# Kernel tuning notes

Hardware: AMD Instinct MI355X
Metric: run time of the kernel (lower is better)

The kernel has to match this reference:

```python
import jax, jax.numpy as jnp
import numpy as np

B = 2048          # number of drug pairs (graphs)
N_PER_DRUG = 32   # nodes per drug subgraph (uniform for static shapes)
F = 128           # node_feature_dim
H = 128           # hidden_dim
E = 1048576       # total edges (~avg degree 8 per node)


def setup_inputs() -> dict:
    key = jax.random.key(0)
    ks = jax.random.split(key, 12)
    total = B * 2 * N_PER_DRUG
    x = jax.random.normal(ks[0], (total, F), dtype=jnp.float32)
    # edges generated within each drug subgraph (2B blocks of N_PER_DRUG nodes)
    blk = jax.random.randint(ks[1], (E,), 0, 2 * B)
    src = blk * N_PER_DRUG + jax.random.randint(ks[2], (E,), 0, N_PER_DRUG)
    dst = blk * N_PER_DRUG + jax.random.randint(ks[3], (E,), 0, N_PER_DRUG)
    edge_index = jnp.stack([src, dst]).astype(jnp.int32)
    ptr = (jnp.arange(B + 1) * 2 * N_PER_DRUG).astype(jnp.int32)
    split = jnp.full((B,), N_PER_DRUG, dtype=jnp.int32)

    def lin(k, shape, fan_in):
        return jax.random.normal(k, shape, dtype=jnp.float32) * (1.0 / np.sqrt(fan_in))

    return {
        "x": x, "edge_index": edge_index, "ptr": ptr, "split": split,
        "W1": lin(ks[4], (F, H), F), "b1": jnp.zeros((H,), jnp.float32),
        "W2": lin(ks[5], (H, H), H), "b2": jnp.zeros((H,), jnp.float32),
        "Wm1": lin(ks[6], (2 * H, H), 2 * H), "bm1": jnp.zeros((H,), jnp.float32),
        "Wm2": lin(ks[7], (H, 1), H), "bm2": jnp.zeros((1,), jnp.float32),
    }


def reference(x, edge_index, ptr, split, W1, b1, W2, b2, Wm1, bm1, Wm2, bm2):
    num_nodes = x.shape[0]
    nB = ptr.shape[0] - 1
    idx = jnp.arange(num_nodes, dtype=jnp.int32)
    g = (jnp.searchsorted(ptr, idx, side="right") - 1).astype(jnp.int32)
    local = idx - ptr[g]
    drug = (local >= split[g]).astype(jnp.int32)
    seg = 2 * g + drug                      # (graph, drug-half) segment id
    src, dst = edge_index[0], edge_index[1]
    # edge valid iff same graph AND same drug half (== the per-sample masks)
    w = (seg[src] == seg[dst]).astype(x.dtype)
    # GCN normalization with self-loops (shared by both layers)
    deg = jax.ops.segment_sum(w, dst, num_segments=num_nodes) + 1.0
    dinv = jax.lax.rsqrt(deg)
    norm = dinv[src] * dinv[dst] * w        # [E]
    self_norm = (dinv * dinv)[:, None]      # [N,1]

    def gcn(h, W, b):
        hw = h @ W
        agg = jax.ops.segment_sum(norm[:, None] * hw[src], dst, num_segments=num_nodes)
        return agg + self_norm * hw + b

    h = jax.nn.relu(gcn(x, W1, b1))
    h = jax.nn.relu(gcn(h, W2, b2))
    nseg = 2 * nB
    cnt = jax.ops.segment_sum(jnp.ones((num_nodes,), x.dtype), seg, num_segments=nseg)
    pooled = jax.ops.segment_sum(h, seg, num_segments=nseg) / jnp.maximum(cnt, 1.0)[:, None]
    pair = jnp.concatenate([pooled[0::2], pooled[1::2]], axis=1)  # [B, 2H]
    z = jax.nn.relu(pair @ Wm1 + bm1) @ Wm2 + bm2
    return jax.nn.sigmoid(z).reshape(-1)
```

## Files before the change

### kernel.cpp

```cpp
#include <hip/hip_runtime.h>
#include <hip/hip_bf16.h>
#include <math.h>

#define NF 128
#define ECAP 512

typedef short bf16x8 __attribute__((ext_vector_type(8)));
typedef float f32x4  __attribute__((ext_vector_type(4)));

union U8 { unsigned u[4]; bf16x8 v; };

__device__ __forceinline__ unsigned pk2(float lo, float hi) {
    union { __hip_bfloat162 h2; unsigned u; } c;
    c.h2 = __float22bfloat162_rn(make_float2(lo, hi));
    return c.u;
}
__device__ __forceinline__ unsigned short f2bf(float f) {
    union { __hip_bfloat16 h; unsigned short u; } c;
    c.h = __float2bfloat16(f);
    return c.u;
}

__global__ void k_prep(const int* __restrict__ ptr, const int* __restrict__ split,
                       int nB, int N, int nseg,
                       unsigned* __restrict__ segloc, int* __restrict__ segstart,
                       int* __restrict__ segcnt, int* __restrict__ cursor,
                       const float* __restrict__ W1, const float* __restrict__ W2,
                       short* __restrict__ Wt1, short* __restrict__ Wt2) {
    int i = blockIdx.x * blockDim.x + threadIdx.x;
    if (i < N) {
        int lo = 0, hi = nB + 1;
        while (lo < hi) { int mid = (lo + hi) >> 1; if (ptr[mid] <= i) lo = mid + 1; else hi = mid; }
        int g = lo - 1;
        int local = i - ptr[g];
        int sp = split[g];
        int drug = (local >= sp) ? 1 : 0;
        int seg = 2 * g + drug;
        int loc = local - (drug ? sp : 0);
        segloc[i] = ((unsigned)seg << 8) | (unsigned)loc;
    }
    if (i < nseg) {
        int g = i >> 1;
        int base = ptr[g];
        int sp = split[g];
        segstart[i] = (i & 1) ? base + sp : base;
        segcnt[i]   = (i & 1) ? (ptr[g + 1] - base - sp) : sp;
        cursor[i]   = 0;
    }
    if (i < 32768) {
        int m = i >> 14;
        int rem = i & 16383;
        int n = rem & 127;
        int k = rem >> 7;
        const float* W = m ? W2 : W1;
        short* Wt = m ? Wt2 : Wt1;
        Wt[n * 128 + k] = (short)f2bf(W[k * 128 + n]);
    }
}

__global__ void __launch_bounds__(1024) k_sort(
    const int* __restrict__ src, const int* __restrict__ dst, int E, int nseg,
    const unsigned* __restrict__ segloc, int* __restrict__ cursor,
    unsigned short* __restrict__ ebuf)
{
    __shared__ unsigned cnt[4096];
    __shared__ unsigned gbase[4096];
    const int t  = threadIdx.x;
    const int e0 = blockIdx.x * 4096;

    for (int i = t; i < 4096; i += 1024) cnt[i] = 0;
    __syncthreads();

    unsigned code[4];
    #pragma unroll
    for (int k = 0; k < 4; ++k) {
        int e = e0 + k * 1024 + t;
        code[k] = 0xFFFFFFFFu;
        if (e < E) {
            unsigned ss = segloc[src[e]], dd = segloc[dst[e]];
            if ((ss >> 8) == (dd >> 8)) {
                code[k] = ((ss >> 8) << 12) | ((dd & 63u) << 6) | (ss & 63u);
                atomicAdd(&cnt[ss >> 8], 1u);
            }
        }
    }
    __syncthreads();

    for (int i = t; i < nseg; i += 1024) {
        unsigned c = cnt[i];
        if (c) gbase[i] = (unsigned)atomicAdd(&cursor[i], (int)c);
    }
    __syncthreads();
    for (int i = t; i < 4096; i += 1024) cnt[i] = 0;
    __syncthreads();

    #pragma unroll
    for (int k = 0; k < 4; ++k) {
        if (code[k] != 0xFFFFFFFFu) {
            unsigned s = code[k] >> 12;
            unsigned pos = gbase[s] + atomicAdd(&cnt[s], 1u);
            if (pos < ECAP)
                ebuf[(s << 9) + pos] = (unsigned short)(code[k] & 0xFFFu);
        }
    }
}

__global__ void __launch_bounds__(64, 3) k_gcn5(
    const float* __restrict__ x,
    const int* __restrict__ segstart, const int* __restrict__ segcnt,
    const int* __restrict__ ecnt, const unsigned short* __restrict__ ebuf,
    const short* __restrict__ Wt1, const float* __restrict__ b1,
    const short* __restrict__ Wt2, const float* __restrict__ b2,
    float* __restrict__ pooled)
{
    __shared__ short xt[128 * 40];
    float* Afp = (float*)xt;
    short* zb  = xt;

    const int seg = blockIdx.x;
    const int l  = threadIdx.x;
    const int fr = l & 15;
    const int g  = l >> 4;
    const int swz = (fr & 7) << 3;

    const int start = segstart[seg];
    const int cnt   = segcnt[seg];

    const int f0 = (l & 7) * 16;
    const int c0 = (l >> 3) * 4;
    float xr[4][16];
    #pragma unroll
    for (int i = 0; i < 4; ++i) {
        if (c0 + i < cnt) {
            const float4* rp = (const float4*)(x + (size_t)(start + c0 + i) * NF + f0);
            float4 a = rp[0], b = rp[1], c = rp[2], d = rp[3];
            xr[i][0]=a.x; xr[i][1]=a.y; xr[i][2]=a.z; xr[i][3]=a.w;
            xr[i][4]=b.x; xr[i][5]=b.y; xr[i][6]=b.z; xr[i][7]=b.w;
            xr[i][8]=c.x; xr[i][9]=c.y; xr[i][10]=c.z; xr[i][11]=c.w;
            xr[i][12]=d.x; xr[i][13]=d.y; xr[i][14]=d.z; xr[i][15]=d.w;
        } else {
            #pragma unroll
            for (int j = 0; j < 16; ++j) xr[i][j] = 0.f;
        }
    }

    for (int i = l; i < 1088; i += 64) Afp[i] = 0.f;
    __syncthreads();

    {
        int en = ecnt[seg];
        en = en < ECAP ? en : ECAP;
        const unsigned short* eb = ebuf + ((size_t)seg << 9);
        for (int i = l; i < en; i += 64) {
            unsigned c = eb[i];
            if ((c & ((32u << 6) | 32u)) == 0u)
                atomicAdd(&Afp[((c >> 6) & 31) * 33 + (c & 31)], 1.0f);
        }
    }
    __syncthreads();

    {
        int r = l & 31, half = l >> 5;
        float s = 0.f;
        const float* row = &Afp[r * 33 + half * 16];
        #pragma unroll
        for (int k = 0; k < 16; ++k) s += row[k];
        s += __shfl_xor(s, 32);
        float dv = rsqrtf(1.0f + s);
        if (l < 32) Afp[1056 + r] = dv;
    }
    __syncthreads();

    bf16x8 bfr0, bfr1;
    {
        float dr0 = Afp[1056 + fr];
        float dr1 = Afp[1056 + 16 + fr];
        float e0[8], e1[8];
        #pragma unroll
        for (int j = 0; j < 8; ++j) {
            int c = g * 8 + j;
            float dc = Afp[1056 + c];
            float v0 = Afp[fr * 33 + c]        * dr0 * dc;
            float v1 = Afp[(16 + fr) * 33 + c] * dr1 * dc;
            if (fr == c)      v0 += dr0 * dr0;
            if (16 + fr == c) v1 += dr1 * dr1;
            e0[j] = v0; e1[j] = v1;
        }
        U8 u0, u1;
        u0.u[0] = pk2(e0[0], e0[1]); u0.u[1] = pk2(e0[2], e0[3]);
        u0.u[2] = pk2(e0[4], e0[5]); u0.u[3] = pk2(e0[6], e0[7]);
        u1.u[0] = pk2(e1[0], e1[1]); u1.u[1] = pk2(e1[2], e1[3]);
        u1.u[2] = pk2(e1[4], e1[5]); u1.u[3] = pk2(e1[6], e1[7]);
        bfr0 = u0.v; bfr1 = u1.v;
    }
    __syncthreads();

    #pragma unroll
    for (int j = 0; j < 16; ++j) {
        uint2 w;
        w.x = pk2(xr[0][j], xr[1][j]);
        w.y = pk2(xr[2][j], xr[3][j]);
        *reinterpret_cast<uint2*>(&xt[(f0 + j) * 40 + c0]) = w;
    }
    __syncthreads();

    for (int layer = 0; layer < 2; ++layer) {
        const short* Wt = layer ? Wt2 : Wt1;
        const float* bb = layer ? b2  : b1;

        unsigned zp[8][4];
        __builtin_amdgcn_s_setprio(1);
        #pragma unroll
        for (int mt = 0; mt < 8; ++mt) {
            bf16x8 af = *(const bf16x8*)&xt[(mt * 16 + fr) * 40 + g * 8];
            f32x4 z0 = {0.f, 0.f, 0.f, 0.f};
            f32x4 z1 = {0.f, 0.f, 0.f, 0.f};
            z0 = __builtin_amdgcn_mfma_f32_16x16x32_bf16(af, bfr0, z0, 0, 0, 0);
            z1 = __builtin_amdgcn_mfma_f32_16x16x32_bf16(af, bfr1, z1, 0, 0, 0);
            zp[mt][0] = pk2(z0[0], z0[1]); zp[mt][1] = pk2(z0[2], z0[3]);
            zp[mt][2] = pk2(z1[0], z1[1]); zp[mt][3] = pk2(z1[2], z1[3]);
        }
        __builtin_amdgcn_s_setprio(0);
        __syncthreads();

        #pragma unroll
        for (int mt = 0; mt < 8; ++mt) {
            int fb = mt * 16 + 4 * g;
            uint2 w0, w1;
            w0.x = zp[mt][0]; w0.y = zp[mt][1];
            w1.x = zp[mt][2]; w1.y = zp[mt][3];
            *reinterpret_cast<uint2*>(&zb[fr * 128 + (fb ^ swz)])        = w0;
            *reinterpret_cast<uint2*>(&zb[(16 + fr) * 128 + (fb ^ swz)]) = w1;
        }
        __syncthreads();

        f32x4 acc[2][8];
        #pragma unroll
        for (int i = 0; i < 2; ++i)
            #pragma unroll
            for (int j = 0; j < 8; ++j) acc[i][j] = (f32x4){0.f, 0.f, 0.f, 0.f};
        #pragma unroll
        for (int kk = 0; kk < 4; ++kk) {
            const int ko = kk * 32 + g * 8;
            bf16x8 a0 = *(const bf16x8*)&zb[fr * 128 + (ko ^ swz)];
            bf16x8 a1 = *(const bf16x8*)&zb[(16 + fr) * 128 + (ko ^ swz)];
            __builtin_amdgcn_s_setprio(1);
            #pragma unroll
            for (int nt = 0; nt < 8; ++nt) {
                bf16x8 wf = *(const bf16x8*)&Wt[(nt * 16 + fr) * 128 + ko];
                acc[0][nt] = __builtin_amdgcn_mfma_f32_16x16x32_bf16(a0, wf, acc[0][nt], 0, 0, 0);
                acc[1][nt] = __builtin_amdgcn_mfma_f32_16x16x32_bf16(a1, wf, acc[1][nt], 0, 0, 0);
            }
            __builtin_amdgcn_s_setprio(0);
        }

        if (layer == 0) {
            __syncthreads();
            #pragma unroll
            for (int nt = 0; nt < 8; ++nt) {
                float bv = bb[nt * 16 + fr];
                #pragma unroll
                for (int mt = 0; mt < 2; ++mt) {
                    float h0 = acc[mt][nt][0] + bv; h0 = h0 > 0.f ? h0 : 0.f;
                    float h1 = acc[mt][nt][1] + bv; h1 = h1 > 0.f ? h1 : 0.f;
                    float h2 = acc[mt][nt][2] + bv; h2 = h2 > 0.f ? h2 : 0.f;
                    float h3 = acc[mt][nt][3] + bv; h3 = h3 > 0.f ? h3 : 0.f;
                    uint2 w;
                    w.x = pk2(h0, h1); w.y = pk2(h2, h3);
                    *reinterpret_cast<uint2*>(&xt[(nt * 16 + fr) * 40 + mt * 16 + 4 * g]) = w;
                }
            }
            __syncthreads();
        } else {
            float rcpc = 1.0f / (float)(cnt > 0 ? cnt : 1);
            #pragma unroll
            for (int nt = 0; nt < 8; ++nt) {
                float bv = bb[nt * 16 + fr];
                float pm = 0.f;
                #pragma unroll
                for (int mt = 0; mt < 2; ++mt)
                    #pragma unroll
                    for (int r = 0; r < 4; ++r) {
                        int node = mt * 16 + 4 * g + r;
                        float h = acc[mt][nt][r] + bv;
                        h = h > 0.f ? h : 0.f;
                        if (node < cnt) pm += h;
                    }
                pm += __shfl_xor(pm, 16);
                pm += __shfl_xor(pm, 32);
                if (l < 16) pooled[(size_t)seg * NF + nt * 16 + l] = pm * rcpc;
            }
        }
    }
}

__global__ void __launch_bounds__(128) k_mlp(
    const float* __restrict__ pooled, const float* __restrict__ Wm1,
    const float* __restrict__ bm1, const float* __restrict__ Wm2,
    const float* __restrict__ bm2, float* __restrict__ out, int nB) {
    __shared__ float pr[4][256];
    __shared__ float red[4][2];
    const int b0 = blockIdx.x * 4;
    const int t = threadIdx.x;

    for (int i = t; i < 1024; i += 128) {
        int p = i >> 8, c = i & 255;
        int pair = b0 + p;
        pr[p][c] = (pair < nB) ? pooled[(size_t)(2 * pair + (c >> 7)) * 128 + (c & 127)] : 0.f;
    }
    __syncthreads();

    float acc0 = bm1[t], acc1 = acc0, acc2 = acc0, acc3 = acc0;
    #pragma unroll 4
    for (int k = 0; k < 256; ++k) {
        float w = Wm1[k * 128 + t];
        acc0 += pr[0][k] * w;
        acc1 += pr[1][k] * w;
        acc2 += pr[2][k] * w;
        acc3 += pr[3][k] * w;
    }
    float wm2 = Wm2[t];
    float v[4];
    v[0] = (acc0 > 0.f ? acc0 : 0.f) * wm2;
    v[1] = (acc1 > 0.f ? acc1 : 0.f) * wm2;
    v[2] = (acc2 > 0.f ? acc2 : 0.f) * wm2;
    v[3] = (acc3 > 0.f ? acc3 : 0.f) * wm2;
    #pragma unroll
    for (int p = 0; p < 4; ++p) {
        #pragma unroll
        for (int o = 32; o > 0; o >>= 1) v[p] += __shfl_xor(v[p], o);
    }
    if ((t & 63) == 0) {
        int w = t >> 6;
        red[0][w] = v[0]; red[1][w] = v[1]; red[2][w] = v[2]; red[3][w] = v[3];
    }
    __syncthreads();
    if (t < 4 && b0 + t < nB) {
        float z = red[t][0] + red[t][1] + bm2[0];
        out[b0 + t] = 1.f / (1.f + expf(-z));
    }
}

static inline size_t alup(size_t v) { return (v + 255) & ~(size_t)255; }

extern "C" void kernel_launch(void* const* d_in, const int* in_sizes, int n_in,
                              void* d_out, int out_size, void* d_ws, size_t ws_size,
                              hipStream_t stream) {
    const float* x     = (const float*)d_in[0];
    const int*   edge  = (const int*)d_in[1];
    const int*   ptr   = (const int*)d_in[2];
    const int*   split = (const int*)d_in[3];
    const float* W1  = (const float*)d_in[4];
    const float* b1  = (const float*)d_in[5];
    const float* W2  = (const float*)d_in[6];
    const float* b2  = (const float*)d_in[7];
    const float* Wm1 = (const float*)d_in[8];
    const float* bm1 = (const float*)d_in[9];
    const float* Wm2 = (const float*)d_in[10];
    const float* bm2 = (const float*)d_in[11];
    float* out = (float*)d_out;

    const int N    = in_sizes[0] / NF;
    const int E    = in_sizes[1] / 2;
    const int nB   = in_sizes[2] - 1;
    const int nseg = 2 * nB;

    char* ws = (char*)d_ws;
    size_t off = 0;
    unsigned*       segloc   = (unsigned*)(ws + off);       off += alup((size_t)N * 4);
    int*            segstart = (int*)(ws + off);            off += alup((size_t)nseg * 4);
    int*            segcnt   = (int*)(ws + off);            off += alup((size_t)nseg * 4);
    int*            cursor   = (int*)(ws + off);            off += alup((size_t)nseg * 4);
    unsigned short* ebuf     = (unsigned short*)(ws + off); off += alup((size_t)nseg * ECAP * 2);
    float*          pooled   = (float*)(ws + off);          off += alup((size_t)nseg * NF * 4);
    short*          Wt1      = (short*)(ws + off);          off += alup(128 * 128 * 2);
    short*          Wt2      = (short*)(ws + off);          off += alup(128 * 128 * 2);

    const int* srcp = edge;
    const int* dstp = edge + E;

    int prepN = N > 32768 ? N : 32768;
    if (prepN < nseg) prepN = nseg;

    k_prep<<<(prepN + 255) / 256, 256, 0, stream>>>(ptr, split, nB, N, nseg,
                                                    segloc, segstart, segcnt, cursor,
                                                    W1, W2, Wt1, Wt2);
    k_sort<<<(E + 4095) / 4096, 1024, 0, stream>>>(srcp, dstp, E, nseg, segloc, cursor, ebuf);
    k_gcn5<<<nseg, 64, 0, stream>>>(x, segstart, segcnt, cursor, ebuf,
                                    Wt1, b1, Wt2, b2, pooled);
    k_mlp<<<(nB + 3) / 4, 128, 0, stream>>>(pooled, Wm1, bm1, Wm2, bm2, out, nB);
}
```

Before: 222.1 us.

## Build per-segment packed 4-bit adjacency via global atomics; split GCN over two waves

After: 241.3 us. 1.09x slower.

```diff
diff --git a/kernel.cpp b/kernel.cpp
--- a/kernel.cpp
+++ b/kernel.cpp
@@ -3,7 +3,6 @@
 #include <math.h>
 
 #define NF 128
-#define ECAP 512
 
 typedef short bf16x8 __attribute__((ext_vector_type(8)));
 typedef float f32x4  __attribute__((ext_vector_type(4)));
@@ -24,7 +23,7 @@
 __global__ void k_prep(const int* __restrict__ ptr, const int* __restrict__ split,
                        int nB, int N, int nseg,
                        unsigned* __restrict__ segloc, int* __restrict__ segstart,
-                       int* __restrict__ segcnt, int* __restrict__ cursor,
+                       int* __restrict__ segcnt,
                        const float* __restrict__ W1, const float* __restrict__ W2,
                        short* __restrict__ Wt1, short* __restrict__ Wt2) {
     int i = blockIdx.x * blockDim.x + threadIdx.x;
@@ -45,7 +44,6 @@
         int sp = split[g];
         segstart[i] = (i & 1) ? base + sp : base;
         segcnt[i]   = (i & 1) ? (ptr[g + 1] - base - sp) : sp;
-        cursor[i]   = 0;
     }
     if (i < 32768) {
         int m = i >> 14;
@@ -58,67 +56,33 @@
     }
 }
 
-__global__ void __launch_bounds__(1024) k_sort(
-    const int* __restrict__ src, const int* __restrict__ dst, int E, int nseg,
-    const unsigned* __restrict__ segloc, int* __restrict__ cursor,
-    unsigned short* __restrict__ ebuf)
-{
-    __shared__ unsigned cnt[4096];
-    __shared__ unsigned gbase[4096];
-    const int t  = threadIdx.x;
-    const int e0 = blockIdx.x * 4096;
-
-    for (int i = t; i < 4096; i += 1024) cnt[i] = 0;
-    __syncthreads();
-
-    unsigned code[4];
-    #pragma unroll
-    for (int k = 0; k < 4; ++k) {
-        int e = e0 + k * 1024 + t;
-        code[k] = 0xFFFFFFFFu;
-        if (e < E) {
-            unsigned ss = segloc[src[e]], dd = segloc[dst[e]];
-            if ((ss >> 8) == (dd >> 8)) {
-                code[k] = ((ss >> 8) << 12) | ((dd & 63u) << 6) | (ss & 63u);
-                atomicAdd(&cnt[ss >> 8], 1u);
-            }
-        }
-    }
-    __syncthreads();
-
-    for (int i = t; i < nseg; i += 1024) {
-        unsigned c = cnt[i];
-        if (c) gbase[i] = (unsigned)atomicAdd(&cursor[i], (int)c);
-    }
-    __syncthreads();
-    for (int i = t; i < 4096; i += 1024) cnt[i] = 0;
-    __syncthreads();
-
-    #pragma unroll
-    for (int k = 0; k < 4; ++k) {
-        if (code[k] != 0xFFFFFFFFu) {
-            unsigned s = code[k] >> 12;
-            unsigned pos = gbase[s] + atomicAdd(&cnt[s], 1u);
-            if (pos < ECAP)
-                ebuf[(s << 9) + pos] = (unsigned short)(code[k] & 0xFFFu);
-        }
-    }
-}
-
-__global__ void __launch_bounds__(64, 3) k_gcn5(
+__global__ void k_cnt(const int* __restrict__ src, const int* __restrict__ dst, int E,
+                      const unsigned* __restrict__ segloc, unsigned* __restrict__ Abits) {
+    int e = blockIdx.x * blockDim.x + threadIdx.x;
+    if (e >= E) return;
+    unsigned ss = segloc[src[e]], dd = segloc[dst[e]];
+    if ((ss >> 8) == (dd >> 8) && ((ss | dd) & 0xE0u) == 0u) {
+        unsigned eidx = (dd & 31u) * 32u + (ss & 31u);
+        atomicAdd(&Abits[(ss >> 8) * 128u + (eidx >> 3)], 1u << (4u * (eidx & 7u)));
+    }
+}
+
+__global__ void __launch_bounds__(128, 6) k_gcn6(
     const float* __restrict__ x,
     const int* __restrict__ segstart, const int* __restrict__ segcnt,
-    const int* __restrict__ ecnt, const unsigned short* __restrict__ ebuf,
+    const unsigned* __restrict__ Abits,
     const short* __restrict__ Wt1, const float* __restrict__ b1,
     const short* __restrict__ Wt2, const float* __restrict__ b2,
     float* __restrict__ pooled)
 {
     __shared__ short xt[128 * 40];
-    float* Afp = (float*)xt;
-    short* zb  = xt;
+    __shared__ float dv[32];
+    short* zb = xt;
 
     const int seg = blockIdx.x;
-    const int l  = threadIdx.x;
+    const int t  = threadIdx.x;
+    const int wv = t >> 6;
+    const int l  = t & 63;
     const int fr = l & 15;
     const int g  = l >> 4;
     const int swz = (fr & 7) << 3;
@@ -126,64 +90,60 @@
     const int start = segstart[seg];
     const int cnt   = segcnt[seg];
 
-    const int f0 = (l & 7) * 16;
-    const int c0 = (l >> 3) * 4;
-    float xr[4][16];
+    const int f0 = (t & 15) * 8;
+    const int c0 = (t >> 4) * 4;
+    float xr[4][8];
     #pragma unroll
     for (int i = 0; i < 4; ++i) {
         if (c0 + i < cnt) {
             const float4* rp = (const float4*)(x + (size_t)(start + c0 + i) * NF + f0);
-            float4 a = rp[0], b = rp[1], c = rp[2], d = rp[3];
+            float4 a = rp[0], b = rp[1];
             xr[i][0]=a.x; xr[i][1]=a.y; xr[i][2]=a.z; xr[i][3]=a.w;
             xr[i][4]=b.x; xr[i][5]=b.y; xr[i][6]=b.z; xr[i][7]=b.w;
-            xr[i][8]=c.x; xr[i][9]=c.y; xr[i][10]=c.z; xr[i][11]=c.w;
-            xr[i][12]=d.x; xr[i][13]=d.y; xr[i][14]=d.z; xr[i][15]=d.w;
         } else {
             #pragma unroll
-            for (int j = 0; j < 16; ++j) xr[i][j] = 0.f;
-        }
-    }
-
-    for (int i = l; i < 1088; i += 64) Afp[i] = 0.f;
-    __syncthreads();
-
-    {
-        int en = ecnt[seg];
-        en = en < ECAP ? en : ECAP;
-        const unsigned short* eb = ebuf + ((size_t)seg << 9);
-        for (int i = l; i < en; i += 64) {
-            unsigned c = eb[i];
-            if ((c & ((32u << 6) | 32u)) == 0u)
-                atomicAdd(&Afp[((c >> 6) & 31) * 33 + (c & 31)], 1.0f);
-        }
-    }
-    __syncthreads();
-
-    {
-        int r = l & 31, half = l >> 5;
-        float s = 0.f;
-        const float* row = &Afp[r * 33 + half * 16];
-        #pragma unroll
-        for (int k = 0; k < 16; ++k) s += row[k];
-        s += __shfl_xor(s, 32);
-        float dv = rsqrtf(1.0f + s);
-        if (l < 32) Afp[1056 + r] = dv;
+            for (int j = 0; j < 8; ++j) xr[i][j] = 0.f;
+        }
+    }
+
+    const unsigned* ab = Abits + (size_t)seg * 128;
+    const unsigned wd0 = ab[fr * 4 + g];
+    const unsigned wd1 = ab[(16 + fr) * 4 + g];
+
+    int s0 = 0, s1 = 0;
+    #pragma unroll
+    for (int j = 0; j < 8; ++j) {
+        s0 += (int)((wd0 >> (4 * j)) & 15u);
+        s1 += (int)((wd1 >> (4 * j)) & 15u);
+    }
+    s0 += __shfl_xor(s0, 16); s0 += __shfl_xor(s0, 32);
+    s1 += __shfl_xor(s1, 16); s1 += __shfl_xor(s1, 32);
+    float dv0 = rsqrtf(1.0f + (float)s0);
+    float dv1 = rsqrtf(1.0f + (float)s1);
+    if (t < 16) { dv[t] = dv0; dv[16 + t] = dv1; }
+
+    #pragma unroll
+    for (int j = 0; j < 8; ++j) {
+        uint2 w;
+        w.x = pk2(xr[0][j], xr[1][j]);
+        w.y = pk2(xr[2][j], xr[3][j]);
+        *reinterpret_cast<uint2*>(&xt[(f0 + j) * 40 + c0]) = w;
     }
     __syncthreads();
 
     bf16x8 bfr0, bfr1;
     {
-        float dr0 = Afp[1056 + fr];
-        float dr1 = Afp[1056 + 16 + fr];
+        float dr0 = dv[fr];
+        float dr1 = dv[16 + fr];
         float e0[8], e1[8];
         #pragma unroll
         for (int j = 0; j < 8; ++j) {
             int c = g * 8 + j;
-            float dc = Afp[1056 + c];
-            float v0 = Afp[fr * 33 + c]        * dr0 * dc;
-            float v1 = Afp[(16 + fr) * 33 + c] * dr1 * dc;
-            if (fr == c)      v0 += dr0 * dr0;
-            if (16 + fr == c) v1 += dr1 * dr1;
+            float dc = dv[c];
+            float v0 = (float)((wd0 >> (4 * j)) & 15u) * dr0 * dc;
+            float v1 = (float)((wd1 >> (4 * j)) & 15u) * dr1 * dc;
+            if (c == fr)      v0 += dr0 * dr0;
+            if (c == 16 + fr) v1 += dr1 * dr1;
             e0[j] = v0; e1[j] = v1;
         }
         U8 u0, u1;
@@ -193,52 +153,43 @@
         u1.u[2] = pk2(e1[4], e1[5]); u1.u[3] = pk2(e1[6], e1[7]);
         bfr0 = u0.v; bfr1 = u1.v;
     }
-    __syncthreads();
-
-    #pragma unroll
-    for (int j = 0; j < 16; ++j) {
-        uint2 w;
-        w.x = pk2(xr[0][j], xr[1][j]);
-        w.y = pk2(xr[2][j], xr[3][j]);
-        *reinterpret_cast<uint2*>(&xt[(f0 + j) * 40 + c0]) = w;
-    }
-    __syncthreads();
 
     for (int layer = 0; layer < 2; ++layer) {
         const short* Wt = layer ? Wt2 : Wt1;
         const float* bb = layer ? b2  : b1;
 
-        unsigned zp[8][4];
+        unsigned zp[4][4];
         __builtin_amdgcn_s_setprio(1);
         #pragma unroll
-        for (int mt = 0; mt < 8; ++mt) {
+        for (int mi = 0; mi < 4; ++mi) {
+            int mt = wv * 4 + mi;
             bf16x8 af = *(const bf16x8*)&xt[(mt * 16 + fr) * 40 + g * 8];
             f32x4 z0 = {0.f, 0.f, 0.f, 0.f};
             f32x4 z1 = {0.f, 0.f, 0.f, 0.f};
             z0 = __builtin_amdgcn_mfma_f32_16x16x32_bf16(af, bfr0, z0, 0, 0, 0);
             z1 = __builtin_amdgcn_mfma_f32_16x16x32_bf16(af, bfr1, z1, 0, 0, 0);
-            zp[mt][0] = pk2(z0[0], z0[1]); zp[mt][1] = pk2(z0[2], z0[3]);
-            zp[mt][2] = pk2(z1[0], z1[1]); zp[mt][3] = pk2(z1[2], z1[3]);
+            zp[mi][0] = pk2(z0[0], z0[1]); zp[mi][1] = pk2(z0[2], z0[3]);
+            zp[mi][2] = pk2(z1[0], z1[1]); zp[mi][3] = pk2(z1[2], z1[3]);
         }
         __builtin_amdgcn_s_setprio(0);
         __syncthreads();
 
         #pragma unroll
-        for (int mt = 0; mt < 8; ++mt) {
-            int fb = mt * 16 + 4 * g;
+        for (int mi = 0; mi < 4; ++mi) {
+            int fb = (wv * 4 + mi) * 16 + 4 * g;
             uint2 w0, w1;
-            w0.x = zp[mt][0]; w0.y = zp[mt][1];
-            w1.x = zp[mt][2]; w1.y = zp[mt][3];
+            w0.x = zp[mi][0]; w0.y = zp[mi][1];
+            w1.x = zp[mi][2]; w1.y = zp[mi][3];
             *reinterpret_cast<uint2*>(&zb[fr * 128 + (fb ^ swz)])        = w0;
             *reinterpret_cast<uint2*>(&zb[(16 + fr) * 128 + (fb ^ swz)]) = w1;
         }
         __syncthreads();
 
-        f32x4 acc[2][8];
+        f32x4 acc[2][4];
         #pragma unroll
         for (int i = 0; i < 2; ++i)
             #pragma unroll
-            for (int j = 0; j < 8; ++j) acc[i][j] = (f32x4){0.f, 0.f, 0.f, 0.f};
+            for (int j = 0; j < 4; ++j) acc[i][j] = (f32x4){0.f, 0.f, 0.f, 0.f};
         #pragma unroll
         for (int kk = 0; kk < 4; ++kk) {
             const int ko = kk * 32 + g * 8;
@@ -246,25 +197,27 @@
             bf16x8 a1 = *(const bf16x8*)&zb[(16 + fr) * 128 + (ko ^ swz)];
             __builtin_amdgcn_s_setprio(1);
             #pragma unroll
-            for (int nt = 0; nt < 8; ++nt) {
+            for (int ni = 0; ni < 4; ++ni) {
+                int nt = wv * 4 + ni;
                 bf16x8 wf = *(const bf16x8*)&Wt[(nt * 16 + fr) * 128 + ko];
-                acc[0][nt] = __builtin_amdgcn_mfma_f32_16x16x32_bf16(a0, wf, acc[0][nt], 0, 0, 0);
-                acc[1][nt] = __builtin_amdgcn_mfma_f32_16x16x32_bf16(a1, wf, acc[1][nt], 0, 0, 0);
+                acc[0][ni] = __builtin_amdgcn_mfma_f32_16x16x32_bf16(a0, wf, acc[0][ni], 0, 0, 0);
+                acc[1][ni] = __builtin_amdgcn_mfma_f32_16x16x32_bf16(a1, wf, acc[1][ni], 0, 0, 0);
             }
             __builtin_amdgcn_s_setprio(0);
         }
+        __syncthreads();
 
         if (layer == 0) {
-            __syncthreads();
-            #pragma unroll
-            for (int nt = 0; nt < 8; ++nt) {
+            #pragma unroll
+            for (int ni = 0; ni < 4; ++ni) {
+                int nt = wv * 4 + ni;
                 float bv = bb[nt * 16 + fr];
                 #pragma unroll
                 for (int mt = 0; mt < 2; ++mt) {
-                    float h0 = acc[mt][nt][0] + bv; h0 = h0 > 0.f ? h0 : 0.f;
-                    float h1 = acc[mt][nt][1] + bv; h1 = h1 > 0.f ? h1 : 0.f;
-                    float h2 = acc[mt][nt][2] + bv; h2 = h2 > 0.f ? h2 : 0.f;
-                    float h3 = acc[mt][nt][3] + bv; h3 = h3 > 0.f ? h3 : 0.f;
+                    float h0 = acc[mt][ni][0] + bv; h0 = h0 > 0.f ? h0 : 0.f;
+                    float h1 = acc[mt][ni][1] + bv; h1 = h1 > 0.f ? h1 : 0.f;
+                    float h2 = acc[mt][ni][2] + bv; h2 = h2 > 0.f ? h2 : 0.f;
+                    float h3 = acc[mt][ni][3] + bv; h3 = h3 > 0.f ? h3 : 0.f;
                     uint2 w;
                     w.x = pk2(h0, h1); w.y = pk2(h2, h3);
                     *reinterpret_cast<uint2*>(&xt[(nt * 16 + fr) * 40 + mt * 16 + 4 * g]) = w;
@@ -274,7 +227,8 @@
         } else {
             float rcpc = 1.0f / (float)(cnt > 0 ? cnt : 1);
             #pragma unroll
-            for (int nt = 0; nt < 8; ++nt) {
+            for (int ni = 0; ni < 4; ++ni) {
+                int nt = wv * 4 + ni;
                 float bv = bb[nt * 16 + fr];
                 float pm = 0.f;
                 #pragma unroll
@@ -282,7 +236,7 @@
                     #pragma unroll
                     for (int r = 0; r < 4; ++r) {
                         int node = mt * 16 + 4 * g + r;
-                        float h = acc[mt][nt][r] + bv;
+                        float h = acc[mt][ni][r] + bv;
                         h = h > 0.f ? h : 0.f;
                         if (node < cnt) pm += h;
                     }
@@ -367,14 +321,13 @@
 
     char* ws = (char*)d_ws;
     size_t off = 0;
-    unsigned*       segloc   = (unsigned*)(ws + off);       off += alup((size_t)N * 4);
-    int*            segstart = (int*)(ws + off);            off += alup((size_t)nseg * 4);
-    int*            segcnt   = (int*)(ws + off);            off += alup((size_t)nseg * 4);
-    int*            cursor   = (int*)(ws + off);            off += alup((size_t)nseg * 4);
-    unsigned short* ebuf     = (unsigned short*)(ws + off); off += alup((size_t)nseg * ECAP * 2);
-    float*          pooled   = (float*)(ws + off);          off += alup((size_t)nseg * NF * 4);
-    short*          Wt1      = (short*)(ws + off);          off += alup(128 * 128 * 2);
-    short*          Wt2      = (short*)(ws + off);          off += alup(128 * 128 * 2);
+    unsigned* segloc   = (unsigned*)(ws + off);  off += alup((size_t)N * 4);
+    int*      segstart = (int*)(ws + off);       off += alup((size_t)nseg * 4);
+    int*      segcnt   = (int*)(ws + off);       off += alup((size_t)nseg * 4);
+    unsigned* Abits    = (unsigned*)(ws + off);  size_t abb = (size_t)nseg * 128 * 4; off += alup(abb);
+    float*    pooled   = (float*)(ws + off);     off += alup((size_t)nseg * NF * 4);
+    short*    Wt1      = (short*)(ws + off);     off += alup(128 * 128 * 2);
+    short*    Wt2      = (short*)(ws + off);     off += alup(128 * 128 * 2);
 
     const int* srcp = edge;
     const int* dstp = edge + E;
@@ -382,11 +335,12 @@
     int prepN = N > 32768 ? N : 32768;
     if (prepN < nseg) prepN = nseg;
 
+    hipMemsetAsync(Abits, 0, abb, stream);
     k_prep<<<(prepN + 255) / 256, 256, 0, stream>>>(ptr, split, nB, N, nseg,
-                                                    segloc, segstart, segcnt, cursor,
+                                                    segloc, segstart, segcnt,
                                                     W1, W2, Wt1, Wt2);
-    k_sort<<<(E + 4095) / 4096, 1024, 0, stream>>>(srcp, dstp, E, nseg, segloc, cursor, ebuf);
-    k_gcn5<<<nseg, 64, 0, stream>>>(x, segstart, segcnt, cursor, ebuf,
-                                    Wt1, b1, Wt2, b2, pooled);
+    k_cnt<<<(E + 255) / 256, 256, 0, stream>>>(srcp, dstp, E, segloc, Abits);
+    k_gcn6<<<nseg, 128, 0, stream>>>(x, segstart, segcnt, Abits,
+                                     Wt1, b1, Wt2, b2, pooled);
     k_mlp<<<(nB + 3) / 4, 128, 0, stream>>>(pooled, Wm1, bm1, Wm2, bm2, out, nB);
 }
```
